# Performance work log

Measured on AMD Instinct MI355X. Metric: run time of the kernel, lower is better.

The kernel has to match this reference:

```python
import jax, jax.numpy as jnp
import numpy as np

V = 30000    # vocab_size
E = 128      # embedding_dim
ENC = 128    # encode_dim
H = 128      # hidden_dim
B = 64       # batch of programs
S = 32       # statements per program (max_len)
K = 64       # AST nodes per statement tree
T = B * S    # statement trees per side
N = T * K    # AST nodes per side
LEVELS = 8   # >= max tree depth (heap layout depth = 6)


def setup_inputs() -> dict:
    key = jax.random.key(0)
    ks = jax.random.split(key, 10)
    # heap-structured trees: node j's parent is (j-1)//2 within its K-node tree
    j = np.tile(np.arange(K), T)
    start = np.repeat(np.arange(T) * K, K)
    parent = np.where(j == 0, N, start + (j - 1) // 2).astype(np.int32)  # roots -> dummy slot N

    def rn(k, shape, scale):
        return jax.random.normal(k, shape, dtype=jnp.float32) * scale

    return {
        "tokens1": jax.random.randint(ks[0], (N,), 0, V, dtype=jnp.int32),
        "parent1": jnp.asarray(parent),
        "tokens2": jax.random.randint(ks[1], (N,), 0, V, dtype=jnp.int32),
        "parent2": jnp.asarray(parent),
        "emb": rn(ks[2], (V, E), 1.0),
        "w_c": rn(ks[3], (ENC, E), E ** -0.5),
        "b_c": jnp.zeros((ENC,), jnp.float32),
        "w_ih_f": rn(ks[4], (3 * H, ENC), ENC ** -0.5),
        "w_hh_f": rn(ks[5], (3 * H, H), H ** -0.5),
        "b_ih_f": jnp.zeros((3 * H,), jnp.float32),
        "b_hh_f": jnp.zeros((3 * H,), jnp.float32),
        "w_ih_b": rn(ks[6], (3 * H, ENC), ENC ** -0.5),
        "w_hh_b": rn(ks[7], (3 * H, H), H ** -0.5),
        "b_ih_b": jnp.zeros((3 * H,), jnp.float32),
        "b_hh_b": jnp.zeros((3 * H,), jnp.float32),
        "w_out": rn(ks[8], (1, H), H ** -0.5),
        "b_out": jnp.zeros((1,), jnp.float32),
    }


def _tree_encode(tokens, parent, emb, w_c, b_c):
    # per-node projection: W_c(embedding(token))  (no activation, as in source)
    base = emb[tokens] @ w_c.T + b_c              # [N, ENC]
    h = base
    for _ in range(LEVELS):                        # level-synchronous subtree sums
        child = jax.ops.segment_sum(h, parent, num_segments=N + 1)[:N]
        h = base + child                           # h_v = base_v + sum_children h_c
    tree_id = jnp.arange(N) // K
    res = jax.ops.segment_max(h, tree_id, num_segments=T)  # [T, ENC]
    return jnp.maximum(res, 0.0)                   # zeros in batch_node join the max


def _gru_scan(xs, h0, w_ih, w_hh, b_ih, b_hh):
    # torch nn.GRU cell math
    def step(h, x_t):
        gi = x_t @ w_ih.T + b_ih
        gh = h @ w_hh.T + b_hh
        i_r, i_z, i_n = jnp.split(gi, 3, axis=-1)
        h_r, h_z, h_n = jnp.split(gh, 3, axis=-1)
        r = jax.nn.sigmoid(i_r + h_r)
        z = jax.nn.sigmoid(i_z + h_z)
        n = jnp.tanh(i_n + r * h_n)
        return (1.0 - z) * n + z * h, None
    h_fin, _ = jax.lax.scan(step, h0, xs)
    return h_fin


def _encode(tokens, parent, emb, w_c, b_c,
            w_ih_f, w_hh_f, b_ih_f, b_hh_f, w_ih_b, w_hh_b, b_ih_b, b_hh_b):
    seq = _tree_encode(tokens, parent, emb, w_c, b_c).reshape(B, S, ENC)
    xs = jnp.transpose(seq, (1, 0, 2))  # [S, B, ENC]
    h0 = jnp.zeros((B, H), seq.dtype)
    hf = _gru_scan(xs, h0, w_ih_f, w_hh_f, b_ih_f, b_hh_f)
    hb = _gru_scan(xs[::-1], h0, w_ih_b, w_hh_b, b_ih_b, b_hh_b)
    return hf + hb                       # pooled program representation [B, H]


def reference(tokens1, parent1, tokens2, parent2, emb, w_c, b_c,
              w_ih_f, w_hh_f, b_ih_f, b_hh_f, w_ih_b, w_hh_b, b_ih_b, b_hh_b,
              w_out, b_out):
    gp = (w_ih_f, w_hh_f, b_ih_f, b_hh_f, w_ih_b, w_hh_b, b_ih_b, b_hh_b)
    lvec = _encode(tokens1, parent1, emb, w_c, b_c, *gp)
    rvec = _encode(tokens2, parent2, emb, w_c, b_c, *gp)
    dist = jnp.abs(lvec - rvec)
    return jax.nn.sigmoid(dist @ w_out.T + b_out)  # [B, 1]
```

## Files before the change

kernel.cpp:

```cpp
#include <hip/hip_runtime.h>
#include <stdint.h>

#define VSZ 30000
#define TPS 2048
#define G3  384

#define OFF_PROJ   0u
#define OFF_WCT    1920000u
#define OFF_SEQ    1936384u
#define OFF_HFIN   2460672u
#define OFF_FRAG   2493440u

using f32x4 = __attribute__((ext_vector_type(4))) float;
using s16x8 = __attribute__((ext_vector_type(8))) short;
union U8 { uint4 u; s16x8 s; };

__device__ __forceinline__ float sigm(float x) { return 1.0f / (1.0f + __expf(-x)); }
__device__ __forceinline__ float tanh_fast(float x) {
  float e = __expf(-2.0f * x);
  return 2.0f / (1.0f + e) - 1.0f;
}
__device__ __forceinline__ unsigned bf16_rn(float f) {
  unsigned u = __float_as_uint(f);
  return (u + 0x7FFFu + ((u >> 16) & 1u)) >> 16;
}

__global__ __launch_bounds__(256) void k_transpose(const float* __restrict__ src,
                                                   float* __restrict__ dst, int R) {
  __shared__ float tile[32][129];
  int r0 = blockIdx.x * 32;
  for (int idx = threadIdx.x; idx < 32 * 128; idx += 256) {
    int r = idx >> 7, c = idx & 127;
    tile[r][c] = src[(r0 + r) * 128 + c];
  }
  __syncthreads();
  for (int idx = threadIdx.x; idx < 32 * 128; idx += 256) {
    int k = idx >> 5, r = idx & 31;
    dst[k * R + r0 + r] = tile[r][k];
  }
}

__global__ __launch_bounds__(256) void k_pack(
    const float* __restrict__ w_ih_f, const float* __restrict__ w_ih_b,
    const float* __restrict__ w_hh_f, const float* __restrict__ w_hh_b,
    uint4* __restrict__ fragimg) {
  int idx = blockIdx.x * 256 + threadIdx.x;
  int l = idx & 63;
  int t = (idx >> 6) & 3;
  int r = idx >> 8;
  int g = r % 3; r /= 3;
  int mat = r & 1; r >>= 1;
  int w = r & 7;
  int dir = r >> 3;
  const float* src = mat ? (dir ? w_hh_b : w_hh_f) : (dir ? w_ih_b : w_ih_f);
  int row = g * 128 + 16 * w + (l & 15);
  int ks  = t * 32 + (l >> 4) * 8;
  float4 f0 = *(const float4*)&src[row * 128 + ks];
  float4 f1 = *(const float4*)&src[row * 128 + ks + 4];
  uint4 u;
  u.x = bf16_rn(f0.x) | (bf16_rn(f0.y) << 16);
  u.y = bf16_rn(f0.z) | (bf16_rn(f0.w) << 16);
  u.z = bf16_rn(f1.x) | (bf16_rn(f1.y) << 16);
  u.w = bf16_rn(f1.z) | (bf16_rn(f1.w) << 16);
  fragimg[idx] = u;
}

__global__ __launch_bounds__(256) void k_proj(const float* __restrict__ emb,
                                              const float* __restrict__ wcT,
                                              const float* __restrict__ b_c,
                                              unsigned short* __restrict__ projb) {
  __shared__ float wT[128 * 128];
  __shared__ float es[32][128];
  int v0 = blockIdx.x * 32;
  for (int idx = threadIdx.x; idx < 128 * 32; idx += 256)
    ((float4*)wT)[idx] = ((const float4*)wcT)[idx];
  for (int idx = threadIdx.x; idx < 32 * 32; idx += 256) {
    int v = idx >> 5;
    float4 val = make_float4(0.f, 0.f, 0.f, 0.f);
    if (v0 + v < VSZ) val = ((const float4*)emb)[v0 * 32 + idx];
    ((float4*)es)[idx] = val;
  }
  __syncthreads();
  int tv = (threadIdx.x >> 5) << 2;
  int te = (threadIdx.x & 31) << 2;
  float4 bc4 = *(const float4*)&b_c[te];
  float4 a0 = bc4, a1 = bc4, a2 = bc4, a3 = bc4;
#pragma unroll 4
  for (int kk = 0; kk < 128; ++kk) {
    float4 w4 = *(float4*)&wT[kk * 128 + te];
    float e0 = es[tv + 0][kk], e1 = es[tv + 1][kk];
    float e2 = es[tv + 2][kk], e3 = es[tv + 3][kk];
    a0.x = fmaf(e0, w4.x, a0.x); a0.y = fmaf(e0, w4.y, a0.y);
    a0.z = fmaf(e0, w4.z, a0.z); a0.w = fmaf(e0, w4.w, a0.w);
    a1.x = fmaf(e1, w4.x, a1.x); a1.y = fmaf(e1, w4.y, a1.y);
    a1.z = fmaf(e1, w4.z, a1.z); a1.w = fmaf(e1, w4.w, a1.w);
    a2.x = fmaf(e2, w4.x, a2.x); a2.y = fmaf(e2, w4.y, a2.y);
    a2.z = fmaf(e2, w4.z, a2.z); a2.w = fmaf(e2, w4.w, a2.w);
    a3.x = fmaf(e3, w4.x, a3.x); a3.y = fmaf(e3, w4.y, a3.y);
    a3.z = fmaf(e3, w4.z, a3.z); a3.w = fmaf(e3, w4.w, a3.w);
  }
#pragma unroll
  for (int i = 0; i < 4; ++i) {
    float4 a = (i == 0) ? a0 : (i == 1) ? a1 : (i == 2) ? a2 : a3;
    int v = v0 + tv + i;
    if (v < VSZ) {
      uint2 u;
      u.x = bf16_rn(a.x) | (bf16_rn(a.y) << 16);
      u.y = bf16_rn(a.z) | (bf16_rn(a.w) << 16);
      *(uint2*)&projb[(size_t)v * 128 + te] = u;
    }
  }
}

__global__ __launch_bounds__(256) void k_tree(const int* __restrict__ tokens1,
                                              const int* __restrict__ tokens2,
                                              const unsigned short* __restrict__ projb,
                                              float* __restrict__ seq) {
  __shared__ int tok[2][64];
  int side = blockIdx.y;
  const int* tokens = side ? tokens2 : tokens1;
  int t0 = blockIdx.x * 2;
  if (threadIdx.x < 128) {
    int tl = threadIdx.x >> 6, j = threadIdx.x & 63;
    tok[tl][j] = tokens[(t0 + tl) * 64 + j];
  }
  __syncthreads();
  int tl = threadIdx.x >> 7;
  int c  = threadIdx.x & 127;
  float s[64];
#pragma unroll
  for (int j = 0; j < 64; ++j)
    s[j] = __uint_as_float(((unsigned)projb[(size_t)tok[tl][j] * 128 + c]) << 16);
  s[31] += s[63];
#pragma unroll
  for (int j = 30; j >= 0; --j) s[j] += s[2 * j + 1] + s[2 * j + 2];
  float m = s[0];
#pragma unroll
  for (int j = 1; j < 64; ++j) m = fmaxf(m, s[j]);
  m = fmaxf(m, 0.0f);
  seq[(size_t)(side * TPS + t0 + tl) * 128 + c] = m;
}

#define KT 1040
#define XS 4160
#define MM(dst, A, B) dst = __builtin_amdgcn_mfma_f32_16x16x32_bf16(A, B, dst, 0, 0, 0)

__global__ __launch_bounds__(512) void k_scan(
    const float* __restrict__ seq,
    const uint4* __restrict__ fragimg,
    const float* __restrict__ b_ih_f, const float* __restrict__ b_ih_b,
    const float* __restrict__ b_hh_f, const float* __restrict__ b_hh_b,
    float* __restrict__ hfin) {
  __shared__ __align__(16) unsigned lds[35360];
  int bx = blockIdx.x;
  int sd = bx & 3, pg = bx >> 2;
  int side = sd >> 1, dir = sd & 1;
  const float* bih = dir ? b_ih_b : b_ih_f;
  const float* bhh = dir ? b_hh_b : b_hh_f;
  int tid = threadIdx.x;
  int w = tid >> 6, l = tid & 63;
  int p  = l & 15;
  int kb = l >> 4;
  int c0 = 16 * w + 4 * kb;

  {
    int pp = tid >> 5, cc = tid & 31;
    int wbyte = (cc >> 3) * KT + (pp + 16 * ((cc & 7) >> 1)) * 16 + (cc & 1) * 8;
    const float* srow = seq + (size_t)(side * TPS + (pg * 16 + pp) * 32) * 128 + 4 * cc;
    for (int ss = 0; ss < 32; ++ss) {
      float4 v = *(const float4*)(srow + (size_t)ss * 128);
      uint2 u;
      u.x = bf16_rn(v.x) | (bf16_rn(v.y) << 16);
      u.y = bf16_rn(v.z) | (bf16_rn(v.w) << 16);
      *(uint2*)((char*)lds + ss * XS + wbyte) = u;
    }
  }
  for (int i = tid; i < 2080; i += 512) lds[32 * 1040 + i] = 0u;

  const uint4* fbase = fragimg + (size_t)(dir * 8 + w) * 1536 + l;
  s16x8 ai[3][4], ah[3][4];
#pragma unroll
  for (int g = 0; g < 3; ++g)
#pragma unroll
    for (int t = 0; t < 4; ++t) {
      U8 u;
      u.u = fbase[g * 256 + t * 64];        ai[g][t] = u.s;
      u.u = fbase[768 + g * 256 + t * 64];  ah[g][t] = u.s;
    }

  f32x4 bir = *(const f32x4*)&bih[c0],       bhr = *(const f32x4*)&bhh[c0];
  f32x4 biz = *(const f32x4*)&bih[128 + c0], bhz = *(const f32x4*)&bhh[128 + c0];
  f32x4 bin = *(const f32x4*)&bih[256 + c0], bhn = *(const f32x4*)&bhh[256 + c0];
  f32x4 bbr = bir + bhr, bbz = biz + bhz;

  int hwb = (c0 >> 5) * KT + (p + 16 * ((c0 & 31) >> 3)) * 16 + (c0 & 7) * 2;

  float hc[4] = {0.f, 0.f, 0.f, 0.f};
  f32x4 z4 = {0.f, 0.f, 0.f, 0.f};
  __syncthreads();

  for (int i = 0; i < 32; ++i) {
    int pos = dir ? (31 - i) : i;
    const char* xb = (const char*)lds + pos * XS;
    const char* hb = (const char*)lds + (32 + (i & 1)) * XS;
    s16x8 xf[4], bf[4];
#pragma unroll
    for (int t = 0; t < 4; ++t) {
      U8 ux; ux.u = *(const uint4*)(xb + t * KT + l * 16); xf[t] = ux.s;
      U8 uh; uh.u = *(const uint4*)(hb + t * KT + l * 16); bf[t] = uh.s;
    }
    f32x4 aR0 = bbr, aR1 = z4, aZ0 = bbz, aZ1 = z4;
    f32x4 aNi0 = bin, aNi1 = z4, aNh0 = bhn, aNh1 = z4;
    MM(aR0,  ai[0][0], xf[0]); MM(aZ0,  ai[1][0], xf[0]); MM(aNi0, ai[2][0], xf[0]);
    MM(aR1,  ai[0][1], xf[1]); MM(aZ1,  ai[1][1], xf[1]); MM(aNi1, ai[2][1], xf[1]);
    MM(aR0,  ai[0][2], xf[2]); MM(aZ0,  ai[1][2], xf[2]); MM(aNi0, ai[2][2], xf[2]);
    MM(aR1,  ai[0][3], xf[3]); MM(aZ1,  ai[1][3], xf[3]); MM(aNi1, ai[2][3], xf[3]);
    MM(aNh0, ah[2][0], bf[0]); MM(aR0,  ah[0][0], bf[0]); MM(aZ0,  ah[1][0], bf[0]);
    MM(aNh1, ah[2][1], bf[1]); MM(aR1,  ah[0][1], bf[1]); MM(aZ1,  ah[1][1], bf[1]);
    MM(aNh0, ah[2][2], bf[2]); MM(aR0,  ah[0][2], bf[2]); MM(aZ0,  ah[1][2], bf[2]);
    MM(aNh1, ah[2][3], bf[3]); MM(aR1,  ah[0][3], bf[3]); MM(aZ1,  ah[1][3], bf[3]);
#pragma unroll
    for (int r4 = 0; r4 < 4; ++r4) {
      float rv = sigm(aR0[r4] + aR1[r4]);
      float zv = sigm(aZ0[r4] + aZ1[r4]);
      float nv = tanh_fast(aNi0[r4] + aNi1[r4] + rv * (aNh0[r4] + aNh1[r4]));
      hc[r4] = (1.0f - zv) * nv + zv * hc[r4];
    }
    uint2 hp;
    hp.x = bf16_rn(hc[0]) | (bf16_rn(hc[1]) << 16);
    hp.y = bf16_rn(hc[2]) | (bf16_rn(hc[3]) << 16);
    *(uint2*)((char*)lds + (32 + ((i + 1) & 1)) * XS + hwb) = hp;
    __syncthreads();
  }
  int scan = sd * 64 + pg * 16 + p;
#pragma unroll
  for (int r4 = 0; r4 < 4; ++r4)
    hfin[(size_t)scan * 128 + c0 + r4] = hc[r4];
}

__global__ __launch_bounds__(64) void k_out(const float* __restrict__ hfin,
                                            const float* __restrict__ w_out,
                                            const float* __restrict__ b_out,
                                            float* __restrict__ out) {
  int b = blockIdx.x, lane = threadIdx.x;
  float p = 0.f;
#pragma unroll
  for (int i = 0; i < 2; ++i) {
    int c = lane + i * 64;
    float l = hfin[(size_t)(0   + b) * 128 + c] + hfin[(size_t)(64  + b) * 128 + c];
    float r = hfin[(size_t)(128 + b) * 128 + c] + hfin[(size_t)(192 + b) * 128 + c];
    p += fabsf(l - r) * w_out[c];
  }
#pragma unroll
  for (int off = 32; off > 0; off >>= 1) p += __shfl_down(p, off);
  if (lane == 0) out[b] = sigm(p + b_out[0]);
}

extern "C" void kernel_launch(void* const* d_in, const int* in_sizes, int n_in,
                              void* d_out, int out_size, void* d_ws, size_t ws_size,
                              hipStream_t stream) {
  (void)in_sizes; (void)n_in; (void)out_size; (void)ws_size;
  const int*   tokens1 = (const int*)d_in[0];
  const int*   tokens2 = (const int*)d_in[2];
  const float* emb     = (const float*)d_in[4];
  const float* w_c     = (const float*)d_in[5];
  const float* b_c     = (const float*)d_in[6];
  const float* w_ih_f  = (const float*)d_in[7];
  const float* w_hh_f  = (const float*)d_in[8];
  const float* b_ih_f  = (const float*)d_in[9];
  const float* b_hh_f  = (const float*)d_in[10];
  const float* w_ih_b  = (const float*)d_in[11];
  const float* w_hh_b  = (const float*)d_in[12];
  const float* b_ih_b  = (const float*)d_in[13];
  const float* b_hh_b  = (const float*)d_in[14];
  const float* w_out   = (const float*)d_in[15];
  const float* b_out   = (const float*)d_in[16];
  float* ws = (float*)d_ws;
  unsigned short* projb = (unsigned short*)(ws + OFF_PROJ);
  float* wcT    = ws + OFF_WCT;
  float* seq    = ws + OFF_SEQ;
  float* hfin   = ws + OFF_HFIN;
  uint4* fragimg = (uint4*)(ws + OFF_FRAG);

  k_transpose<<<4, 256, 0, stream>>>(w_c, wcT, 128);
  k_pack<<<96, 256, 0, stream>>>(w_ih_f, w_ih_b, w_hh_f, w_hh_b, fragimg);
  k_proj<<<(VSZ + 31) / 32, 256, 0, stream>>>(emb, wcT, b_c, projb);
  k_tree<<<dim3(TPS / 2, 2), 256, 0, stream>>>(tokens1, tokens2, projb, seq);
  k_scan<<<16, 512, 0, stream>>>(seq, fragimg, b_ih_f, b_ih_b, b_hh_f, b_hh_b, hfin);
  k_out<<<64, 64, 0, stream>>>(hfin, w_out, b_out, (float*)d_out);
}
```

Measured before the change: 115.8 us.

## Use bf16 MFMA for vocab projection, drop transpose kernel, widen tree blocks

The vocabulary projection (emb @ w_c^T over 30000 rows) is rewritten to use bf16 MFMA 16x16x32 instructions. Embedding tiles are converted to bf16 in LDS, and W_c fragments are built directly in registers, which removes the separate transpose kernel and its workspace buffer. The tree kernel now handles four trees per 512-thread block instead of two. This cuts FP32 FMA work and one kernel launch, at the cost of rounding embeddings and weights to bf16 before the matmul.

```diff
diff --git a/kernel.cpp b/kernel.cpp
--- a/kernel.cpp
+++ b/kernel.cpp
@@ -6,10 +6,9 @@
 #define G3  384
 
 #define OFF_PROJ   0u
-#define OFF_WCT    1920000u
-#define OFF_SEQ    1936384u
-#define OFF_HFIN   2460672u
-#define OFF_FRAG   2493440u
+#define OFF_SEQ    1920000u
+#define OFF_HFIN   2444288u
+#define OFF_FRAG   2477056u
 
 using f32x4 = __attribute__((ext_vector_type(4))) float;
 using s16x8 = __attribute__((ext_vector_type(8))) short;
@@ -25,20 +24,9 @@
   return (u + 0x7FFFu + ((u >> 16) & 1u)) >> 16;
 }
 
-__global__ __launch_bounds__(256) void k_transpose(const float* __restrict__ src,
-                                                   float* __restrict__ dst, int R) {
-  __shared__ float tile[32][129];
-  int r0 = blockIdx.x * 32;
-  for (int idx = threadIdx.x; idx < 32 * 128; idx += 256) {
-    int r = idx >> 7, c = idx & 127;
-    tile[r][c] = src[(r0 + r) * 128 + c];
-  }
-  __syncthreads();
-  for (int idx = threadIdx.x; idx < 32 * 128; idx += 256) {
-    int k = idx >> 5, r = idx & 31;
-    dst[k * R + r0 + r] = tile[r][k];
-  }
-}
+#define KT 1040
+#define XS 4160
+#define MM(dst, A, B) dst = __builtin_amdgcn_mfma_f32_16x16x32_bf16(A, B, dst, 0, 0, 0)
 
 __global__ __launch_bounds__(256) void k_pack(
     const float* __restrict__ w_ih_f, const float* __restrict__ w_ih_b,
@@ -65,62 +53,74 @@
   fragimg[idx] = u;
 }
 
-__global__ __launch_bounds__(256) void k_proj(const float* __restrict__ emb,
-                                              const float* __restrict__ wcT,
+__global__ __launch_bounds__(512) void k_proj(const float* __restrict__ emb,
+                                              const float* __restrict__ w_c,
                                               const float* __restrict__ b_c,
                                               unsigned short* __restrict__ projb) {
-  __shared__ float wT[128 * 128];
-  __shared__ float es[32][128];
-  int v0 = blockIdx.x * 32;
-  for (int idx = threadIdx.x; idx < 128 * 32; idx += 256)
-    ((float4*)wT)[idx] = ((const float4*)wcT)[idx];
-  for (int idx = threadIdx.x; idx < 32 * 32; idx += 256) {
-    int v = idx >> 5;
-    float4 val = make_float4(0.f, 0.f, 0.f, 0.f);
-    if (v0 + v < VSZ) val = ((const float4*)emb)[v0 * 32 + idx];
-    ((float4*)es)[idx] = val;
-  }
+  __shared__ __align__(16) char blds[8 * XS];
+  int tid = threadIdx.x;
+  int v0 = blockIdx.x * 128;
+  {
+    int pp = tid >> 5, cc = tid & 31;
+    int wbyte = (cc >> 3) * KT + (pp + 16 * ((cc & 7) >> 1)) * 16 + (cc & 1) * 8;
+    for (int nt = 0; nt < 8; ++nt) {
+      int row = v0 + nt * 16 + pp;
+      float4 v = make_float4(0.f, 0.f, 0.f, 0.f);
+      if (row < VSZ) v = *(const float4*)&emb[(size_t)row * 128 + 4 * cc];
+      uint2 u;
+      u.x = bf16_rn(v.x) | (bf16_rn(v.y) << 16);
+      u.y = bf16_rn(v.z) | (bf16_rn(v.w) << 16);
+      *(uint2*)(blds + nt * XS + wbyte) = u;
+    }
+  }
+  int w = tid >> 6, l = tid & 63;
+  s16x8 af[4];
+  {
+    int row = 16 * w + (l & 15);
+    int kb = (l >> 4) * 8;
+#pragma unroll
+    for (int t = 0; t < 4; ++t) {
+      float4 f0 = *(const float4*)&w_c[row * 128 + t * 32 + kb];
+      float4 f1 = *(const float4*)&w_c[row * 128 + t * 32 + kb + 4];
+      U8 u;
+      u.u.x = bf16_rn(f0.x) | (bf16_rn(f0.y) << 16);
+      u.u.y = bf16_rn(f0.z) | (bf16_rn(f0.w) << 16);
+      u.u.z = bf16_rn(f1.x) | (bf16_rn(f1.y) << 16);
+      u.u.w = bf16_rn(f1.z) | (bf16_rn(f1.w) << 16);
+      af[t] = u.s;
+    }
+  }
+  f32x4 bias = *(const f32x4*)&b_c[16 * w + (l >> 4) * 4];
   __syncthreads();
-  int tv = (threadIdx.x >> 5) << 2;
-  int te = (threadIdx.x & 31) << 2;
-  float4 bc4 = *(const float4*)&b_c[te];
-  float4 a0 = bc4, a1 = bc4, a2 = bc4, a3 = bc4;
-#pragma unroll 4
-  for (int kk = 0; kk < 128; ++kk) {
-    float4 w4 = *(float4*)&wT[kk * 128 + te];
-    float e0 = es[tv + 0][kk], e1 = es[tv + 1][kk];
-    float e2 = es[tv + 2][kk], e3 = es[tv + 3][kk];
-    a0.x = fmaf(e0, w4.x, a0.x); a0.y = fmaf(e0, w4.y, a0.y);
-    a0.z = fmaf(e0, w4.z, a0.z); a0.w = fmaf(e0, w4.w, a0.w);
-    a1.x = fmaf(e1, w4.x, a1.x); a1.y = fmaf(e1, w4.y, a1.y);
-    a1.z = fmaf(e1, w4.z, a1.z); a1.w = fmaf(e1, w4.w, a1.w);
-    a2.x = fmaf(e2, w4.x, a2.x); a2.y = fmaf(e2, w4.y, a2.y);
-    a2.z = fmaf(e2, w4.z, a2.z); a2.w = fmaf(e2, w4.w, a2.w);
-    a3.x = fmaf(e3, w4.x, a3.x); a3.y = fmaf(e3, w4.y, a3.y);
-    a3.z = fmaf(e3, w4.z, a3.z); a3.w = fmaf(e3, w4.w, a3.w);
-  }
-#pragma unroll
-  for (int i = 0; i < 4; ++i) {
-    float4 a = (i == 0) ? a0 : (i == 1) ? a1 : (i == 2) ? a2 : a3;
-    int v = v0 + tv + i;
+  for (int nt = 0; nt < 8; ++nt) {
+    s16x8 bf[4];
+#pragma unroll
+    for (int t = 0; t < 4; ++t) {
+      U8 u; u.u = *(const uint4*)(blds + nt * XS + t * KT + l * 16);
+      bf[t] = u.s;
+    }
+    f32x4 acc = bias;
+    MM(acc, af[0], bf[0]); MM(acc, af[1], bf[1]);
+    MM(acc, af[2], bf[2]); MM(acc, af[3], bf[3]);
+    int v = v0 + nt * 16 + (l & 15);
     if (v < VSZ) {
       uint2 u;
-      u.x = bf16_rn(a.x) | (bf16_rn(a.y) << 16);
-      u.y = bf16_rn(a.z) | (bf16_rn(a.w) << 16);
-      *(uint2*)&projb[(size_t)v * 128 + te] = u;
-    }
-  }
-}
-
-__global__ __launch_bounds__(256) void k_tree(const int* __restrict__ tokens1,
+      u.x = bf16_rn(acc[0]) | (bf16_rn(acc[1]) << 16);
+      u.y = bf16_rn(acc[2]) | (bf16_rn(acc[3]) << 16);
+      *(uint2*)&projb[(size_t)v * 128 + 16 * w + (l >> 4) * 4] = u;
+    }
+  }
+}
+
+__global__ __launch_bounds__(512) void k_tree(const int* __restrict__ tokens1,
                                               const int* __restrict__ tokens2,
                                               const unsigned short* __restrict__ projb,
                                               float* __restrict__ seq) {
-  __shared__ int tok[2][64];
+  __shared__ int tok[4][64];
   int side = blockIdx.y;
   const int* tokens = side ? tokens2 : tokens1;
-  int t0 = blockIdx.x * 2;
-  if (threadIdx.x < 128) {
+  int t0 = blockIdx.x * 4;
+  if (threadIdx.x < 256) {
     int tl = threadIdx.x >> 6, j = threadIdx.x & 63;
     tok[tl][j] = tokens[(t0 + tl) * 64 + j];
   }
@@ -140,10 +140,6 @@
   m = fmaxf(m, 0.0f);
   seq[(size_t)(side * TPS + t0 + tl) * 128 + c] = m;
 }
-
-#define KT 1040
-#define XS 4160
-#define MM(dst, A, B) dst = __builtin_amdgcn_mfma_f32_16x16x32_bf16(A, B, dst, 0, 0, 0)
 
 __global__ __launch_bounds__(512) void k_scan(
     const float* __restrict__ seq,
@@ -277,15 +273,13 @@
   const float* b_out   = (const float*)d_in[16];
   float* ws = (float*)d_ws;
   unsigned short* projb = (unsigned short*)(ws + OFF_PROJ);
-  float* wcT    = ws + OFF_WCT;
   float* seq    = ws + OFF_SEQ;
   float* hfin   = ws + OFF_HFIN;
   uint4* fragimg = (uint4*)(ws + OFF_FRAG);
 
-  k_transpose<<<4, 256, 0, stream>>>(w_c, wcT, 128);
   k_pack<<<96, 256, 0, stream>>>(w_ih_f, w_ih_b, w_hh_f, w_hh_b, fragimg);
-  k_proj<<<(VSZ + 31) / 32, 256, 0, stream>>>(emb, wcT, b_c, projb);
-  k_tree<<<dim3(TPS / 2, 2), 256, 0, stream>>>(tokens1, tokens2, projb, seq);
+  k_proj<<<(VSZ + 127) / 128, 512, 0, stream>>>(emb, w_c, b_c, projb);
+  k_tree<<<dim3(TPS / 4, 2), 512, 0, stream>>>(tokens1, tokens2, projb, seq);
   k_scan<<<16, 512, 0, stream>>>(seq, fragimg, b_ih_f, b_ih_b, b_hh_f, b_hh_b, hfin);
   k_out<<<64, 64, 0, stream>>>(hfin, w_out, b_out, (float*)d_out);
 }
```

After: 95.94 us, median of 2. -17.2%, faster.
